# Performance work log

Measured on AMD Instinct MI355X. Metric: run time of the kernel, lower is better.

The kernel has to match this reference:

```python
import jax, jax.numpy as jnp
import numpy as np

N = 50000   # nodes
E = 800000  # edges (avg degree 16)
R = 3       # relations (distance bins)
IN = 3      # node_input_dim
H = 64      # hidden_dim
EA = 6      # edge_input_dim
DH = 32     # decoder_hidden_dim


def setup_inputs() -> dict:
    key = jax.random.key(0)
    ks = jax.random.split(key, 16)
    x = jax.random.normal(ks[0], (N, IN), jnp.float32)
    edge_index = jax.random.randint(ks[1], (2, E), 0, N)
    edge_attr = jax.random.uniform(ks[2], (E, EA), dtype=jnp.float32)
    # scale log1p-distance column so edges span all 3 bins (thresholds ~8.52, ~9.21)
    edge_attr = edge_attr.at[:, 0].mul(12.0)
    p = lambda k, s: jax.random.normal(k, s, jnp.float32) * 0.1
    return dict(
        x=x, edge_index=edge_index, edge_attr=edge_attr,
        w0=p(ks[3], (R, IN, H)), root0=p(ks[4], (IN, H)), b0=jnp.zeros((H,), jnp.float32),
        w1=p(ks[5], (R, H, H)),  root1=p(ks[6], (H, H)),  b1=jnp.zeros((H,), jnp.float32),
        w2=p(ks[7], (R, H, H)),  root2=p(ks[8], (H, H)),  b2=jnp.zeros((H,), jnp.float32),
        ln_g0=jnp.ones((H,), jnp.float32), ln_b0=jnp.zeros((H,), jnp.float32),
        ln_g1=jnp.ones((H,), jnp.float32), ln_b1=jnp.zeros((H,), jnp.float32),
        ln_g2=jnp.ones((H,), jnp.float32), ln_b2=jnp.zeros((H,), jnp.float32),
        res_w=p(ks[9], (IN, H)), res_b=jnp.zeros((H,), jnp.float32),
        dec_w1=p(ks[10], (4 * H + EA, DH)), dec_b1=jnp.zeros((DH,), jnp.float32),
        dec_w2=p(ks[11], (DH, DH // 2)),    dec_b2=jnp.zeros((DH // 2,), jnp.float32),
        dec_w3=p(ks[12], (DH // 2, 1)),     dec_b3=jnp.zeros((1,), jnp.float32),
    )


def _layernorm(v, g, b, eps=1e-5):
    mu = v.mean(-1, keepdims=True)
    var = ((v - mu) ** 2).mean(-1, keepdims=True)
    return (v - mu) / jnp.sqrt(var + eps) * g + b


def reference(x, edge_index, edge_attr,
              w0, root0, b0, w1, root1, b1, w2, root2, b2,
              ln_g0, ln_b0, ln_g1, ln_b1, ln_g2, ln_b2,
              res_w, res_b,
              dec_w1, dec_b1, dec_w2, dec_b2, dec_w3, dec_b3):
    dist = edge_attr[:, 0]
    q1 = jnp.log1p(jnp.float32(5000.0))
    q2 = jnp.log1p(jnp.float32(10000.0))
    edge_type = (dist > q1).astype(jnp.int32) + (dist > q2).astype(jnp.int32)  # [E]
    src, dst = edge_index[0], edge_index[1]

    def rgcn(xi, W, root, b):
        # RGCNConv with per-relation mean aggregation:
        # out_i = root x_i + b + sum_r W_r * mean_{j in N_r(i)} x_j
        # aggregate-then-transform: segment-sum masked source feats, divide by
        # per-relation in-degree, then one small [in,H] matmul per relation.
        xs = xi[src]                                  # [E, in] gather
        out = xi @ root + b                           # [N, H]
        for r in range(R):
            m = (edge_type == r).astype(xi.dtype)[:, None]
            s = jax.ops.segment_sum(xs * m, dst, num_segments=N)   # [N, in]
            c = jax.ops.segment_sum(m, dst, num_segments=N)        # [N, 1]
            out = out + (s / jnp.maximum(c, 1.0)) @ W[r]
        return out

    # encoder (eval mode -> dropout is identity)
    h = jax.nn.relu(rgcn(x, w0, root0, b0))
    h1 = _layernorm(h + x @ res_w + res_b, ln_g0, ln_b0)
    h = jax.nn.relu(rgcn(h1, w1, root1, b1))
    h2 = _layernorm(h + h1, ln_g1, ln_b1)
    h = jax.nn.relu(rgcn(h2, w2, root2, b2))
    h3 = _layernorm(h + h2, ln_g2, ln_b2)

    # edge decoder
    hs, hd = h3[src], h3[dst]                         # [E, H] gathers
    dec_in = jnp.concatenate([hs, hd, jnp.abs(hs - hd), hs * hd, edge_attr], axis=-1)
    z = jax.nn.relu(dec_in @ dec_w1 + dec_b1)
    z = jax.nn.relu(z @ dec_w2 + dec_b2)
    return (z @ dec_w3 + dec_b3).squeeze(-1)          # [E]
```

## Files before the change

kernel.cpp:

```cpp
#include <hip/hip_runtime.h>
#include <math.h>

#define NN 50000
#define NE 800000
#define HD 64
#define NB 196
#define NBK 196
#define BSE 2048
#define DT 5

typedef float f32x4 __attribute__((ext_vector_type(4)));
typedef float f32x16 __attribute__((ext_vector_type(16)));
typedef short short8 __attribute__((ext_vector_type(8)));
typedef _Float16 hf2 __attribute__((ext_vector_type(2)));
typedef _Float16 half8 __attribute__((ext_vector_type(8)));

__device__ __forceinline__ float wave_sum(float v) {
  #pragma unroll
  for (int off = 32; off > 0; off >>= 1) v += __shfl_xor(v, off, 64);
  return v;
}

__device__ __forceinline__ unsigned f2h_pk(float a, float b) {
  auto v = __builtin_amdgcn_cvt_pkrtz(a, b);
  union { decltype(v) h; unsigned u; } cv; cv.h = v; return cv.u;
}
__device__ __forceinline__ unsigned short f2h(float a) {
  union { _Float16 h; unsigned short u; } cv; cv.h = (_Float16)a; return cv.u;
}
__device__ __forceinline__ float h2f(unsigned short b) {
  union { unsigned short u; _Float16 h; } v; v.u = b; return (float)v.h;
}

__global__ __launch_bounds__(256) void bucket_count(
    const int* __restrict__ ei, int* __restrict__ bcnt)
{
  __shared__ int h[NBK];
  for (int i = threadIdx.x; i < NBK; i += 256) h[i] = 0;
  __syncthreads();
  int e0 = blockIdx.x * BSE;
  #pragma unroll
  for (int k = 0; k < BSE / 256; k++) {
    int e = e0 + k * 256 + threadIdx.x;
    if (e < NE) atomicAdd(&h[ei[NE + e] >> 8], 1);
  }
  __syncthreads();
  for (int i = threadIdx.x; i < NBK; i += 256)
    if (h[i]) atomicAdd(&bcnt[i], h[i]);
}

__global__ __launch_bounds__(256) void bucket_scan(
    const int* __restrict__ bcnt, int* __restrict__ bbase, int* __restrict__ bcur)
{
  __shared__ int sd[256];
  int v = (threadIdx.x < NBK) ? bcnt[threadIdx.x] : 0;
  sd[threadIdx.x] = v;
  __syncthreads();
  for (int s = 1; s < 256; s <<= 1) {
    int t = (threadIdx.x >= s) ? sd[threadIdx.x - s] : 0;
    __syncthreads();
    sd[threadIdx.x] += t;
    __syncthreads();
  }
  if (threadIdx.x < NBK) {
    int ex = sd[threadIdx.x] - v;
    bbase[threadIdx.x] = ex;
    bcur[threadIdx.x] = ex;
  }
  if (threadIdx.x == 0) bbase[NBK] = NE;
}

__global__ __launch_bounds__(256) void bucket_scatter(
    const int* __restrict__ ei, const float* __restrict__ ea,
    int* __restrict__ bcur, unsigned* __restrict__ recs)
{
  __shared__ int hcnt[NBK], hbase[NBK];
  for (int i = threadIdx.x; i < NBK; i += 256) hcnt[i] = 0;
  __syncthreads();
  const float q1 = log1pf(5000.0f);
  const float q2 = log1pf(10000.0f);
  int e0 = blockIdx.x * BSE;
  unsigned rec[BSE / 256];
  int bk[BSE / 256];
  #pragma unroll
  for (int k = 0; k < BSE / 256; k++) {
    int e = e0 + k * 256 + threadIdx.x;
    bk[k] = -1;
    if (e < NE) {
      int s = ei[e], d = ei[NE + e];
      float dist = ea[(size_t)e * 6];
      int r = (dist > q1 ? 1 : 0) + (dist > q2 ? 1 : 0);
      rec[k] = (unsigned)s | ((unsigned)(d & 255) << 16) | ((unsigned)r << 24);
      bk[k] = d >> 8;
      atomicAdd(&hcnt[bk[k]], 1);
    }
  }
  __syncthreads();
  for (int i = threadIdx.x; i < NBK; i += 256) {
    hbase[i] = hcnt[i] ? atomicAdd(&bcur[i], hcnt[i]) : 0;
    hcnt[i] = 0;
  }
  __syncthreads();
  #pragma unroll
  for (int k = 0; k < BSE / 256; k++) {
    if (bk[k] >= 0) {
      int idx = atomicAdd(&hcnt[bk[k]], 1);
      recs[hbase[bk[k]] + idx] = rec[k];
    }
  }
}

__global__ __launch_bounds__(256) void bucket_hist(
    const unsigned* __restrict__ recs, const int* __restrict__ bbase,
    int* __restrict__ cntR)
{
  __shared__ int h[768];
  for (int i = threadIdx.x; i < 768; i += 256) h[i] = 0;
  __syncthreads();
  int b = blockIdx.x;
  int lo = bbase[b], hi = bbase[b + 1];
  for (int i = lo + threadIdx.x; i < hi; i += 256) {
    unsigned rec = recs[i];
    int dlow = (rec >> 16) & 255, r = (rec >> 24) & 3;
    atomicAdd(&h[dlow * 3 + r], 1);
  }
  __syncthreads();
  for (int i = threadIdx.x; i < 768; i += 256) {
    int n = b * 256 + i / 3;
    if (n < NN) cntR[n * 3 + i % 3] = h[i];
  }
}

__global__ __launch_bounds__(256) void bucket_place(
    const unsigned* __restrict__ recs, const int* __restrict__ bbase,
    const int* __restrict__ off3, unsigned short* __restrict__ sorted)
{
  __shared__ int cur[768];
  int b = blockIdx.x;
  for (int i = threadIdx.x; i < 768; i += 256) {
    int n = b * 256 + i / 3;
    cur[i] = (n < NN) ? off3[n * 3 + i % 3] : 0;
  }
  __syncthreads();
  int lo = bbase[b], hi = bbase[b + 1];
  for (int i = lo + threadIdx.x; i < hi; i += 256) {
    unsigned rec = recs[i];
    int s = rec & 0xFFFF, dlow = (rec >> 16) & 255, r = (rec >> 24) & 3;
    int pos = atomicAdd(&cur[dlow * 3 + r], 1);
    sorted[pos] = (unsigned short)s;
  }
}

__global__ __launch_bounds__(256) void scanA(const int* __restrict__ cntR, int* __restrict__ bsum) {
  __shared__ int sd[256];
  int n = blockIdx.x * 256 + threadIdx.x;
  int deg = 0;
  if (n < NN) deg = cntR[3 * n] + cntR[3 * n + 1] + cntR[3 * n + 2];
  sd[threadIdx.x] = deg;
  __syncthreads();
  #pragma unroll
  for (int s = 128; s > 0; s >>= 1) {
    if (threadIdx.x < s) sd[threadIdx.x] += sd[threadIdx.x + s];
    __syncthreads();
  }
  if (threadIdx.x == 0) bsum[blockIdx.x] = sd[0];
}

__global__ __launch_bounds__(256) void scanB(int* __restrict__ bsum) {
  __shared__ int sd[256];
  int v = (threadIdx.x < NB) ? bsum[threadIdx.x] : 0;
  sd[threadIdx.x] = v;
  __syncthreads();
  for (int s = 1; s < 256; s <<= 1) {
    int t = (threadIdx.x >= s) ? sd[threadIdx.x - s] : 0;
    __syncthreads();
    sd[threadIdx.x] += t;
    __syncthreads();
  }
  if (threadIdx.x < NB) bsum[threadIdx.x] = sd[threadIdx.x] - v;
}

__global__ __launch_bounds__(256) void scanC(
    const int* __restrict__ cntR, const int* __restrict__ bsum,
    int* __restrict__ off3, float* __restrict__ dinv)
{
  __shared__ int sd[256];
  int n = blockIdx.x * 256 + threadIdx.x;
  int c0 = 0, c1 = 0, c2 = 0;
  if (n < NN) { c0 = cntR[3 * n]; c1 = cntR[3 * n + 1]; c2 = cntR[3 * n + 2]; }
  int deg = c0 + c1 + c2;
  sd[threadIdx.x] = deg;
  __syncthreads();
  for (int s = 1; s < 256; s <<= 1) {
    int t = (threadIdx.x >= s) ? sd[threadIdx.x - s] : 0;
    __syncthreads();
    sd[threadIdx.x] += t;
    __syncthreads();
  }
  if (n < NN) {
    int o = bsum[blockIdx.x] + sd[threadIdx.x] - deg;
    off3[3 * n + 0] = o;
    off3[3 * n + 1] = o + c0;
    off3[3 * n + 2] = o + c0 + c1;
    dinv[3 * n + 0] = 1.0f / (float)(c0 > 1 ? c0 : 1);
    dinv[3 * n + 1] = 1.0f / (float)(c1 > 1 ? c1 : 1);
    dinv[3 * n + 2] = 1.0f / (float)(c2 > 1 ? c2 : 1);
  }
}

__global__ __launch_bounds__(256) void agg0_pack(
    const float* __restrict__ x, const int* __restrict__ off3, const int* __restrict__ cntR,
    const unsigned short* __restrict__ sorted, float* __restrict__ agg0,
    const float* __restrict__ W1, const float* __restrict__ W2,
    const float* __restrict__ root1, const float* __restrict__ w1,
    const float* __restrict__ root2, const float* __restrict__ w2,
    unsigned short* __restrict__ pk3, unsigned short* __restrict__ pk2,
    unsigned short* __restrict__ pkl1, unsigned short* __restrict__ pkl2)
{
  if (blockIdx.x < 3) {
    if (blockIdx.x == 0) {
      for (int idx = threadIdx.x; idx < 8704; idx += 256) {
        int j = idx & 7, l = (idx >> 3) & 63, t = idx >> 9;
        int k = 16 * t + 8 * (l >> 5) + j;
        int n = l & 31;
        pk3[idx] = (k < 262) ? f2h(W1[k * 32 + n]) : (unsigned short)0;
      }
      for (int idx = threadIdx.x; idx < 512; idx += 256) {
        int j = idx & 7, l = idx >> 3;
        int k = (l >> 4) * 8 + j, n = l & 15;
        pk2[idx] = f2h(W2[k * 16 + n]);
      }
    } else {
      const float* root = (blockIdx.x == 1) ? root1 : root2;
      const float* W    = (blockIdx.x == 1) ? w1 : w2;
      unsigned short* pkL = (blockIdx.x == 1) ? pkl1 : pkl2;
      for (int idx = threadIdx.x; idx < 16384; idx += 256) {
        int j = idx & 7, l = (idx >> 3) & 63, nt = (idx >> 9) & 3, t = idx >> 11;
        int k = t * 32 + (l >> 4) * 8 + j;
        int n = nt * 16 + (l & 15);
        float w = (k < 64) ? root[k * 64 + n]
                           : W[((k - 64) >> 6) * 4096 + (k & 63) * 64 + n];
        pkL[idx] = f2h(w);
      }
    }
    return;
  }
  int wid = ((blockIdx.x - 3) * blockDim.x + threadIdx.x) >> 6;
  int lane = threadIdx.x & 63;
  int n = wid * 16 + (lane >> 2);
  int f = lane & 3;
  if (n >= NN) return;
  #pragma unroll
  for (int r = 0; r < 3; r++) {
    int st = off3[3 * n + r], len = cntR[3 * n + r];
    float a = 0.f;
    int i = 0;
    for (; i + 4 <= len; i += 4) {
      int s0 = sorted[st + i], s1 = sorted[st + i + 1];
      int s2 = sorted[st + i + 2], s3 = sorted[st + i + 3];
      float v0 = (f < 3) ? x[s0 * 3 + f] : 0.f;
      float v1 = (f < 3) ? x[s1 * 3 + f] : 0.f;
      float v2 = (f < 3) ? x[s2 * 3 + f] : 0.f;
      float v3 = (f < 3) ? x[s3 * 3 + f] : 0.f;
      a += (v0 + v1) + (v2 + v3);
    }
    for (; i < len; i++) {
      int s0 = sorted[st + i];
      a += (f < 3) ? x[s0 * 3 + f] : 0.f;
    }
    if (f < 3) agg0[n * 9 + r * 3 + f] = a;
  }
}

__global__ __launch_bounds__(256) void node0_kernel(
    const float* __restrict__ x, const float* __restrict__ agg0, const float* __restrict__ dinv,
    const float* __restrict__ w0, const float* __restrict__ root0, const float* __restrict__ b0,
    const float* __restrict__ res_w, const float* __restrict__ res_b,
    const float* __restrict__ g, const float* __restrict__ bb,
    unsigned short* __restrict__ hb)
{
  int wid = __builtin_amdgcn_readfirstlane((int)((blockIdx.x * blockDim.x + threadIdx.x) >> 6));
  int lane = threadIdx.x & 63;
  int n0 = wid * 8;
  if (n0 >= NN) return;
  float wr[3], ww[9], wres[3];
  #pragma unroll
  for (int i = 0; i < 3; i++) { wr[i] = root0[i * HD + lane]; wres[i] = res_w[i * HD + lane]; }
  #pragma unroll
  for (int i = 0; i < 9; i++) ww[i] = w0[i * HD + lane];
  float vb = b0[lane], vrb = res_b[lane], vg = g[lane], vbb = bb[lane];
  #pragma unroll
  for (int k = 0; k < 8; k++) {
    int nk = n0 + k;
    float xv[3];
    #pragma unroll
    for (int i = 0; i < 3; i++) xv[i] = x[nk * 3 + i];
    float v = vb;
    #pragma unroll
    for (int i = 0; i < 3; i++) v = fmaf(xv[i], wr[i], v);
    #pragma unroll
    for (int r = 0; r < 3; r++) {
      float s = 0.f;
      #pragma unroll
      for (int i = 0; i < 3; i++) s = fmaf(agg0[nk * 9 + r * 3 + i], ww[r * 3 + i], s);
      v = fmaf(dinv[nk * 3 + r], s, v);
    }
    v = fmaxf(v, 0.f);
    float res = vrb;
    #pragma unroll
    for (int i = 0; i < 3; i++) res = fmaf(xv[i], wres[i], res);
    float t = v + res;
    float mu = wave_sum(t) * 0.015625f;
    float dt = t - mu;
    float var = wave_sum(dt * dt) * 0.015625f;
    float o = dt * rsqrtf(var + 1e-5f) * vg + vbb;
    hb[(size_t)nk * HD + lane] = f2h(o);
  }
}

__global__ __launch_bounds__(256) void layer_fused(
    const unsigned short* __restrict__ hb_in, const unsigned short* __restrict__ pkL,
    const float* __restrict__ bias, const float* __restrict__ g, const float* __restrict__ bb,
    const int* __restrict__ off3, const int* __restrict__ cntR,
    const unsigned short* __restrict__ sorted, const float* __restrict__ dinv,
    unsigned short* __restrict__ hb_out)
{
  __shared__ unsigned short tile[4][16][256];
  int wv = threadIdx.x >> 6;
  int lane = threadIdx.x & 63;
  int wid = (blockIdx.x * blockDim.x + threadIdx.x) >> 6;
  int n0 = wid * 16;
  if (n0 >= NN) return;
  char* T = (char*)&tile[wv][0][0];

  {
    int m = lane >> 2;
    int q = lane & 3;
    int node = n0 + m;
    int swz = (m & 7) << 4;
    const unsigned short* hrow = hb_in + (size_t)node * HD + q * 16;
    uint4 rv0 = *(const uint4*)(hrow);
    uint4 rv1 = *(const uint4*)(hrow + 8);
    *(uint4*)(T + m * 512 + ((q * 32) ^ swz))      = rv0;
    *(uint4*)(T + m * 512 + ((q * 32 + 16) ^ swz)) = rv1;

    union U4 { uint4 u; hf2 h[4]; };
    #pragma unroll
    for (int r = 0; r < 3; r++) {
      int st = off3[node * 3 + r];
      int len = cntR[node * 3 + r];
      hf2 acc[8];
      #pragma unroll
      for (int j = 0; j < 8; j++) acc[j] = (hf2){(_Float16)0.f, (_Float16)0.f};
      int i = 0;
      for (; i + 4 <= len; i += 4) {
        int s0 = sorted[st + i],     s1 = sorted[st + i + 1];
        int s2 = sorted[st + i + 2], s3 = sorted[st + i + 3];
        const uint4* p0 = (const uint4*)(hb_in + (size_t)s0 * HD + q * 16);
        const uint4* p1 = (const uint4*)(hb_in + (size_t)s1 * HD + q * 16);
        const uint4* p2 = (const uint4*)(hb_in + (size_t)s2 * HD + q * 16);
        const uint4* p3 = (const uint4*)(hb_in + (size_t)s3 * HD + q * 16);
        U4 a0, a1, b0, b1, c0, c1, d0, d1;
        a0.u = p0[0]; a1.u = p0[1];
        b0.u = p1[0]; b1.u = p1[1];
        c0.u = p2[0]; c1.u = p2[1];
        d0.u = p3[0]; d1.u = p3[1];
        #pragma unroll
        for (int k = 0; k < 4; k++) {
          acc[k]     += (a0.h[k] + b0.h[k]) + (c0.h[k] + d0.h[k]);
          acc[4 + k] += (a1.h[k] + b1.h[k]) + (c1.h[k] + d1.h[k]);
        }
      }
      for (; i < len; i++) {
        int s0 = sorted[st + i];
        const uint4* p0 = (const uint4*)(hb_in + (size_t)s0 * HD + q * 16);
        U4 u0, u1;
        u0.u = p0[0]; u1.u = p0[1];
        #pragma unroll
        for (int k = 0; k < 4; k++) {
          acc[k]     += u0.h[k];
          acc[4 + k] += u1.h[k];
        }
      }
      float dv = dinv[node * 3 + r];
      unsigned pk[8];
      #pragma unroll
      for (int j = 0; j < 8; j++)
        pk[j] = f2h_pk((float)acc[j][0] * dv, (float)acc[j][1] * dv);
      uint4 w0 = make_uint4(pk[0], pk[1], pk[2], pk[3]);
      uint4 w1 = make_uint4(pk[4], pk[5], pk[6], pk[7]);
      *(uint4*)(T + m * 512 + ((128 + r * 128 + q * 32) ^ swz))      = w0;
      *(uint4*)(T + m * 512 + ((128 + r * 128 + q * 32 + 16) ^ swz)) = w1;
    }
  }

  asm volatile("s_waitcnt lgkmcnt(0)" ::: "memory");
  __builtin_amdgcn_sched_barrier(0);

  int m2 = lane & 15, gq = lane >> 4;
  int swz2 = (m2 & 7) << 4;
  const half8* Bp = (const half8*)pkL;
  f32x4 acc[4];
  #pragma unroll
  for (int nt = 0; nt < 4; nt++) acc[nt] = (f32x4){0.f, 0.f, 0.f, 0.f};
  #pragma unroll
  for (int t = 0; t < 8; t++) {
    union AF { short8 s; half8 h; } af;
    af.s = *(const short8*)(T + m2 * 512 + ((gq * 16 + t * 64) ^ swz2));
    #pragma unroll
    for (int nt = 0; nt < 4; nt++)
      acc[nt] = __builtin_amdgcn_mfma_f32_16x16x32_f16(af.h, Bp[(t * 4 + nt) * 64 + lane], acc[nt], 0, 0, 0);
  }

  float bias_v[4], g_v[4], bb_v[4];
  #pragma unroll
  for (int nt = 0; nt < 4; nt++) {
    bias_v[nt] = bias[nt * 16 + m2];
    g_v[nt] = g[nt * 16 + m2];
    bb_v[nt] = bb[nt * 16 + m2];
  }
  #pragma unroll
  for (int rr = 0; rr < 4; rr++) {
    int lrow = gq * 4 + rr;
    int nodeo = n0 + lrow;
    int swzr = (lrow & 7) << 4;
    float tv[4], s = 0.f;
    #pragma unroll
    for (int nt = 0; nt < 4; nt++) {
      unsigned short rh = *(const unsigned short*)(T + lrow * 512 + (((nt * 16 + m2) * 2) ^ swzr));
      float res = h2f(rh);
      float v = fmaxf(acc[nt][rr] + bias_v[nt], 0.f) + res;
      tv[nt] = v; s += v;
    }
    #pragma unroll
    for (int o = 1; o < 16; o <<= 1) s += __shfl_xor(s, o, 64);
    float mu = s * 0.015625f;
    float s2 = 0.f;
    #pragma unroll
    for (int nt = 0; nt < 4; nt++) { float dd = tv[nt] - mu; s2 += dd * dd; }
    #pragma unroll
    for (int o = 1; o < 16; o <<= 1) s2 += __shfl_xor(s2, o, 64);
    float rstd = rsqrtf(s2 * 0.015625f + 1e-5f);
    #pragma unroll
    for (int nt = 0; nt < 4; nt++) {
      float o = (tv[nt] - mu) * rstd * g_v[nt] + bb_v[nt];
      hb_out[(size_t)nodeo * HD + nt * 16 + m2] = f2h(o);
    }
  }
}

__global__ __launch_bounds__(256) void decoder_mfma(
    const unsigned short* __restrict__ hb, const int* __restrict__ ei, const float* __restrict__ ea,
    const unsigned short* __restrict__ pk3, const unsigned short* __restrict__ pk2,
    const float* __restrict__ B1, const float* __restrict__ B2,
    const float* __restrict__ W3, const float* __restrict__ B3,
    float* __restrict__ out)
{
  __shared__ float Zl[4 * 32 * 33];
  __shared__ unsigned short Bsh[8704 + 512];
  {
    unsigned* dsh = (unsigned*)Bsh;
    const unsigned* sp3 = (const unsigned*)pk3;
    for (int i = threadIdx.x; i < 4352; i += 256) dsh[i] = sp3[i];
    const unsigned* sp2 = (const unsigned*)pk2;
    if (threadIdx.x < 256) dsh[4352 + threadIdx.x] = sp2[threadIdx.x];
  }
  __syncthreads();

  int wv = threadIdx.x >> 6;
  int lane = threadIdx.x & 63;
  int r = lane & 31, u = lane >> 5;
  int base = (blockIdx.x * 4 + wv) * 32 * DT;

  int m = lane & 15, g = lane >> 4;
  float b1v = B1[r];
  float bias2 = B2[m];
  float w3v = W3[m];
  float b3v = B3[0];
  float* Z = Zl + wv * 1056;
  const half8* Bp  = (const half8*)Bsh;
  const half8* Bp2 = (const half8*)(Bsh + 8704);

  union u8h { short8 s8; half8 h8; hf2 h[4]; unsigned w[4]; };

  u8h hsA[4], hdA[4], hsB[4], hdB[4];
  float2 E0[3], E1[3], E2[3];

  auto GATH = [&](u8h* Hs, u8h* Hd, int s, int d) {
    const unsigned short* ps = hb + (size_t)s * HD + u * 8;
    const unsigned short* pq = hb + (size_t)d * HD + u * 8;
    #pragma unroll
    for (int t = 0; t < 4; t++) {
      Hs[t].s8 = *(const short8*)(ps + t * 16);
      Hd[t].s8 = *(const short8*)(pq + t * 16);
    }
  };
  auto LDEA = [&](float2* E, int e0t) {
    if (u == 0) {
      const float* er = ea + (size_t)(e0t + r) * 6;
      E[0] = *(const float2*)(er);
      E[1] = *(const float2*)(er + 2);
      E[2] = *(const float2*)(er + 4);
    }
  };
  auto COMP = [&](u8h* Hs, u8h* Hd, float2* E, int e0t) {
    u8h ad[4], pd[4];
    #pragma unroll
    for (int t = 0; t < 4; t++) {
      #pragma unroll
      for (int k = 0; k < 4; k++) {
        union { hf2 h; unsigned u; } dd;
        dd.h = Hs[t].h[k] - Hd[t].h[k];
        ad[t].w[k] = dd.u & 0x7FFF7FFFu;
        pd[t].h[k] = Hs[t].h[k] * Hd[t].h[k];
      }
    }
    u8h aea;
    aea.w[0] = 0; aea.w[1] = 0; aea.w[2] = 0; aea.w[3] = 0;
    if (u == 0) {
      aea.w[0] = f2h_pk(E[0].x, E[0].y);
      aea.w[1] = f2h_pk(E[1].x, E[1].y);
      aea.w[2] = f2h_pk(E[2].x, E[2].y);
    }

    f32x16 acc = {0.f, 0.f, 0.f, 0.f, 0.f, 0.f, 0.f, 0.f,
                  0.f, 0.f, 0.f, 0.f, 0.f, 0.f, 0.f, 0.f};
    #pragma unroll
    for (int t = 0; t < 4; t++)
      acc = __builtin_amdgcn_mfma_f32_32x32x16_f16(Hs[t].h8, Bp[t * 64 + lane], acc, 0, 0, 0);
    #pragma unroll
    for (int t = 0; t < 4; t++)
      acc = __builtin_amdgcn_mfma_f32_32x32x16_f16(Hd[t].h8, Bp[(4 + t) * 64 + lane], acc, 0, 0, 0);
    #pragma unroll
    for (int t = 0; t < 4; t++)
      acc = __builtin_amdgcn_mfma_f32_32x32x16_f16(ad[t].h8, Bp[(8 + t) * 64 + lane], acc, 0, 0, 0);
    #pragma unroll
    for (int t = 0; t < 4; t++)
      acc = __builtin_amdgcn_mfma_f32_32x32x16_f16(pd[t].h8, Bp[(12 + t) * 64 + lane], acc, 0, 0, 0);
    acc = __builtin_amdgcn_mfma_f32_32x32x16_f16(aea.h8, Bp[16 * 64 + lane], acc, 0, 0, 0);

    #pragma unroll
    for (int i = 0; i < 16; i++) {
      int row = (i & 3) + 8 * (i >> 2) + 4 * u;
      Z[r * 33 + row] = fmaxf(acc[i] + b1v, 0.f);
    }

    #pragma unroll
    for (int q = 0; q < 2; q++) {
      u8h A2;
      #pragma unroll
      for (int j2 = 0; j2 < 4; j2++)
        A2.w[j2] = f2h_pk(Z[(g * 8 + 2 * j2) * 33 + q * 16 + m],
                          Z[(g * 8 + 2 * j2 + 1) * 33 + q * 16 + m]);
      f32x4 acc2 = {0.f, 0.f, 0.f, 0.f};
      acc2 = __builtin_amdgcn_mfma_f32_16x16x32_f16(A2.h8, Bp2[lane], acc2, 0, 0, 0);

      float t0 = fmaxf(acc2[0] + bias2, 0.f) * w3v;
      float t1 = fmaxf(acc2[1] + bias2, 0.f) * w3v;
      float t2 = fmaxf(acc2[2] + bias2, 0.f) * w3v;
      float t3 = fmaxf(acc2[3] + bias2, 0.f) * w3v;
      #pragma unroll
      for (int off = 1; off < 16; off <<= 1) {
        t0 += __shfl_xor(t0, off, 64);
        t1 += __shfl_xor(t1, off, 64);
        t2 += __shfl_xor(t2, off, 64);
        t3 += __shfl_xor(t3, off, 64);
      }
      if (m < 4) {
        float val = (m == 0) ? t0 : (m == 1) ? t1 : (m == 2) ? t2 : t3;
        out[e0t + q * 16 + g * 4 + m] = val + b3v;
      }
    }
  };

  int s1, d1;
  {
    int s0 = ei[base + r], d0 = ei[NE + base + r];
    LDEA(E0, base);
    GATH(hsA, hdA, s0, d0);
  }
  s1 = ei[base + 32 + r]; d1 = ei[NE + base + 32 + r];
  LDEA(E1, base + 32);

  #pragma unroll
  for (int t = 0; t < DT; t++) {
    if (t + 1 < DT) GATH(hsB, hdB, s1, d1);
    int s2 = 0, d2 = 0;
    if (t + 2 < DT) {
      s2 = ei[base + (t + 2) * 32 + r]; d2 = ei[NE + base + (t + 2) * 32 + r];
      LDEA(E2, base + (t + 2) * 32);
    }
    COMP(hsA, hdA, E0, base + t * 32);
    #pragma unroll
    for (int k = 0; k < 4; k++) { hsA[k] = hsB[k]; hdA[k] = hdB[k]; }
    E0[0] = E1[0]; E0[1] = E1[1]; E0[2] = E1[2];
    E1[0] = E2[0]; E1[1] = E2[1]; E1[2] = E2[2];
    s1 = s2; d1 = d2;
  }
}

extern "C" void kernel_launch(void* const* d_in, const int* in_sizes, int n_in,
                              void* d_out, int out_size, void* d_ws, size_t ws_size,
                              hipStream_t stream) {
  const float* x      = (const float*)d_in[0];
  const int*   ei     = (const int*)d_in[1];
  const float* ea     = (const float*)d_in[2];
  const float* w0     = (const float*)d_in[3];
  const float* root0  = (const float*)d_in[4];
  const float* b0     = (const float*)d_in[5];
  const float* w1     = (const float*)d_in[6];
  const float* root1  = (const float*)d_in[7];
  const float* b1     = (const float*)d_in[8];
  const float* w2     = (const float*)d_in[9];
  const float* root2  = (const float*)d_in[10];
  const float* b2     = (const float*)d_in[11];
  const float* ln_g0  = (const float*)d_in[12];
  const float* ln_b0  = (const float*)d_in[13];
  const float* ln_g1  = (const float*)d_in[14];
  const float* ln_b1  = (const float*)d_in[15];
  const float* ln_g2  = (const float*)d_in[16];
  const float* ln_b2  = (const float*)d_in[17];
  const float* res_w  = (const float*)d_in[18];
  const float* res_b  = (const float*)d_in[19];
  const float* dec_w1 = (const float*)d_in[20];
  const float* dec_b1 = (const float*)d_in[21];
  const float* dec_w2 = (const float*)d_in[22];
  const float* dec_b2 = (const float*)d_in[23];
  const float* dec_w3 = (const float*)d_in[24];
  const float* dec_b3 = (const float*)d_in[25];

  char* ws = (char*)d_ws;
  unsigned* recs = (unsigned*)(ws + 0);
  int*   bcnt    = (int*)(ws + 3200000);
  int*   bbase   = (int*)(ws + 3201024);
  int*   bcur    = (int*)(ws + 3202048);
  float* agg0    = (float*)(ws + 3203072);
  int*   bsum    = (int*)(ws + 5003072);
  int*   off3    = (int*)(ws + 5004096);
  float* dinv    = (float*)(ws + 5604096);
  int*   cntR    = (int*)(ws + 6204096);
  unsigned short* sorted = (unsigned short*)(ws + 6804096);
  unsigned short* pk3  = (unsigned short*)(ws + 8404096);
  unsigned short* pkw2 = (unsigned short*)(ws + 8421504);
  unsigned short* pkl1 = (unsigned short*)(ws + 8422528);
  unsigned short* pkl2 = (unsigned short*)(ws + 8455296);
  unsigned short* hb   = (unsigned short*)(ws + 8488064);
  unsigned short* hb2  = (unsigned short*)(ws + 14888064);

  hipMemsetAsync(bcnt, 0, 1024, stream);

  const int sort_blocks = (NE + BSE - 1) / BSE;

  bucket_count<<<sort_blocks, 256, 0, stream>>>(ei, bcnt);
  bucket_scan<<<1, 256, 0, stream>>>(bcnt, bbase, bcur);
  bucket_scatter<<<sort_blocks, 256, 0, stream>>>(ei, ea, bcur, recs);
  bucket_hist<<<NBK, 256, 0, stream>>>(recs, bbase, cntR);
  scanA<<<NB, 256, 0, stream>>>(cntR, bsum);
  scanB<<<1, 256, 0, stream>>>(bsum);
  scanC<<<NB, 256, 0, stream>>>(cntR, bsum, off3, dinv);
  bucket_place<<<NBK, 256, 0, stream>>>(recs, bbase, off3, sorted);

  agg0_pack<<<3 + (NN + 63) / 64, 256, 0, stream>>>(x, off3, cntR, sorted, agg0,
                                                    dec_w1, dec_w2, root1, w1, root2, w2,
                                                    pk3, pkw2, pkl1, pkl2);

  const int node0_blocks = (NN / 8 + 3) / 4;
  const int fused_blocks = (NN / 16 + 3) / 4;

  node0_kernel<<<node0_blocks, 256, 0, stream>>>(x, agg0, dinv, w0, root0, b0,
                                                 res_w, res_b, ln_g0, ln_b0, hb);

  layer_fused<<<fused_blocks, 256, 0, stream>>>(hb, pkl1, b1, ln_g1, ln_b1,
                                                off3, cntR, sorted, dinv, hb2);
  layer_fused<<<fused_blocks, 256, 0, stream>>>(hb2, pkl2, b2, ln_g2, ln_b2,
                                                off3, cntR, sorted, dinv, hb);

  decoder_mfma<<<NE / (128 * DT), 256, 0, stream>>>(hb, ei, ea, pk3, pkw2, dec_b1,
                                                    dec_b2, dec_w3, dec_b3, (float*)d_out);
}
```

Before: 273.8 us.

## Fuse CSR build kernels, widen gather unroll, store decoder hidden as fp16

Merges bucket_hist, three scan kernels and bucket_place into one kernel per bucket. Each bucket computes a local prefix sum offset from the bucket base, which removes four launches and the global scan round-trips. The neighbour-aggregation loop in layer_fused now issues 8 gathers per iteration instead of 4, to raise memory-level parallelism. The decoder stores its first hidden layer in LDS as packed fp16 instead of fp32, with a launch-bounds occupancy hint, to cut LDS traffic and conversions; the wider unroll may add register pressure.

```diff
diff --git a/kernel.cpp b/kernel.cpp
--- a/kernel.cpp
+++ b/kernel.cpp
@@ -4,7 +4,6 @@
 #define NN 50000
 #define NE 800000
 #define HD 64
-#define NB 196
 #define NBK 196
 #define BSE 2048
 #define DT 5
@@ -110,101 +109,54 @@
   }
 }
 
-__global__ __launch_bounds__(256) void bucket_hist(
+__global__ __launch_bounds__(256) void bucket_histplace(
     const unsigned* __restrict__ recs, const int* __restrict__ bbase,
-    int* __restrict__ cntR)
+    int* __restrict__ cntR, int* __restrict__ off3, float* __restrict__ dinv,
+    unsigned short* __restrict__ sorted)
 {
   __shared__ int h[768];
-  for (int i = threadIdx.x; i < 768; i += 256) h[i] = 0;
-  __syncthreads();
+  __shared__ int cur[768];
+  __shared__ int ts[256];
   int b = blockIdx.x;
+  int t = threadIdx.x;
+  for (int i = t; i < 768; i += 256) h[i] = 0;
+  __syncthreads();
   int lo = bbase[b], hi = bbase[b + 1];
-  for (int i = lo + threadIdx.x; i < hi; i += 256) {
+  for (int i = lo + t; i < hi; i += 256) {
     unsigned rec = recs[i];
-    int dlow = (rec >> 16) & 255, r = (rec >> 24) & 3;
-    atomicAdd(&h[dlow * 3 + r], 1);
-  }
-  __syncthreads();
-  for (int i = threadIdx.x; i < 768; i += 256) {
-    int n = b * 256 + i / 3;
-    if (n < NN) cntR[n * 3 + i % 3] = h[i];
-  }
-}
-
-__global__ __launch_bounds__(256) void bucket_place(
-    const unsigned* __restrict__ recs, const int* __restrict__ bbase,
-    const int* __restrict__ off3, unsigned short* __restrict__ sorted)
-{
-  __shared__ int cur[768];
-  int b = blockIdx.x;
-  for (int i = threadIdx.x; i < 768; i += 256) {
-    int n = b * 256 + i / 3;
-    cur[i] = (n < NN) ? off3[n * 3 + i % 3] : 0;
-  }
-  __syncthreads();
-  int lo = bbase[b], hi = bbase[b + 1];
-  for (int i = lo + threadIdx.x; i < hi; i += 256) {
+    atomicAdd(&h[((rec >> 16) & 255) * 3 + ((rec >> 24) & 3)], 1);
+  }
+  __syncthreads();
+  int s0 = h[3 * t], s1 = h[3 * t + 1], s2 = h[3 * t + 2];
+  int tot = s0 + s1 + s2;
+  ts[t] = tot;
+  __syncthreads();
+  for (int s = 1; s < 256; s <<= 1) {
+    int v = (t >= s) ? ts[t - s] : 0;
+    __syncthreads();
+    ts[t] += v;
+    __syncthreads();
+  }
+  int base = lo + ts[t] - tot;
+  int n = b * 256 + t;
+  if (n < NN) {
+    off3[3 * n + 0] = base;
+    off3[3 * n + 1] = base + s0;
+    off3[3 * n + 2] = base + s0 + s1;
+    cntR[3 * n + 0] = s0;
+    cntR[3 * n + 1] = s1;
+    cntR[3 * n + 2] = s2;
+    dinv[3 * n + 0] = 1.0f / (float)(s0 > 1 ? s0 : 1);
+    dinv[3 * n + 1] = 1.0f / (float)(s1 > 1 ? s1 : 1);
+    dinv[3 * n + 2] = 1.0f / (float)(s2 > 1 ? s2 : 1);
+  }
+  cur[3 * t] = base; cur[3 * t + 1] = base + s0; cur[3 * t + 2] = base + s0 + s1;
+  __syncthreads();
+  for (int i = lo + t; i < hi; i += 256) {
     unsigned rec = recs[i];
-    int s = rec & 0xFFFF, dlow = (rec >> 16) & 255, r = (rec >> 24) & 3;
-    int pos = atomicAdd(&cur[dlow * 3 + r], 1);
-    sorted[pos] = (unsigned short)s;
-  }
-}
-
-__global__ __launch_bounds__(256) void scanA(const int* __restrict__ cntR, int* __restrict__ bsum) {
-  __shared__ int sd[256];
-  int n = blockIdx.x * 256 + threadIdx.x;
-  int deg = 0;
-  if (n < NN) deg = cntR[3 * n] + cntR[3 * n + 1] + cntR[3 * n + 2];
-  sd[threadIdx.x] = deg;
-  __syncthreads();
-  #pragma unroll
-  for (int s = 128; s > 0; s >>= 1) {
-    if (threadIdx.x < s) sd[threadIdx.x] += sd[threadIdx.x + s];
-    __syncthreads();
-  }
-  if (threadIdx.x == 0) bsum[blockIdx.x] = sd[0];
-}
-
-__global__ __launch_bounds__(256) void scanB(int* __restrict__ bsum) {
-  __shared__ int sd[256];
-  int v = (threadIdx.x < NB) ? bsum[threadIdx.x] : 0;
-  sd[threadIdx.x] = v;
-  __syncthreads();
-  for (int s = 1; s < 256; s <<= 1) {
-    int t = (threadIdx.x >= s) ? sd[threadIdx.x - s] : 0;
-    __syncthreads();
-    sd[threadIdx.x] += t;
-    __syncthreads();
-  }
-  if (threadIdx.x < NB) bsum[threadIdx.x] = sd[threadIdx.x] - v;
-}
-
-__global__ __launch_bounds__(256) void scanC(
-    const int* __restrict__ cntR, const int* __restrict__ bsum,
-    int* __restrict__ off3, float* __restrict__ dinv)
-{
-  __shared__ int sd[256];
-  int n = blockIdx.x * 256 + threadIdx.x;
-  int c0 = 0, c1 = 0, c2 = 0;
-  if (n < NN) { c0 = cntR[3 * n]; c1 = cntR[3 * n + 1]; c2 = cntR[3 * n + 2]; }
-  int deg = c0 + c1 + c2;
-  sd[threadIdx.x] = deg;
-  __syncthreads();
-  for (int s = 1; s < 256; s <<= 1) {
-    int t = (threadIdx.x >= s) ? sd[threadIdx.x - s] : 0;
-    __syncthreads();
-    sd[threadIdx.x] += t;
-    __syncthreads();
-  }
-  if (n < NN) {
-    int o = bsum[blockIdx.x] + sd[threadIdx.x] - deg;
-    off3[3 * n + 0] = o;
-    off3[3 * n + 1] = o + c0;
-    off3[3 * n + 2] = o + c0 + c1;
-    dinv[3 * n + 0] = 1.0f / (float)(c0 > 1 ? c0 : 1);
-    dinv[3 * n + 1] = 1.0f / (float)(c1 > 1 ? c1 : 1);
-    dinv[3 * n + 2] = 1.0f / (float)(c2 > 1 ? c2 : 1);
+    int idx = ((rec >> 16) & 255) * 3 + ((rec >> 24) & 3);
+    int pos = atomicAdd(&cur[idx], 1);
+    sorted[pos] = (unsigned short)(rec & 0xFFFF);
   }
 }
 
@@ -353,25 +305,37 @@
       #pragma unroll
       for (int j = 0; j < 8; j++) acc[j] = (hf2){(_Float16)0.f, (_Float16)0.f};
       int i = 0;
-      for (; i + 4 <= len; i += 4) {
-        int s0 = sorted[st + i],     s1 = sorted[st + i + 1];
-        int s2 = sorted[st + i + 2], s3 = sorted[st + i + 3];
+      for (; i + 8 <= len; i += 8) {
+        int ss[8];
+        #pragma unroll
+        for (int j = 0; j < 8; j++) ss[j] = sorted[st + i + j];
+        U4 lo[8], hiw[8];
+        #pragma unroll
+        for (int j = 0; j < 8; j++) {
+          const uint4* p = (const uint4*)(hb_in + (size_t)ss[j] * HD + q * 16);
+          lo[j].u = p[0]; hiw[j].u = p[1];
+        }
+        #pragma unroll
+        for (int k = 0; k < 4; k++) {
+          acc[k]     += ((lo[0].h[k] + lo[1].h[k]) + (lo[2].h[k] + lo[3].h[k]))
+                      + ((lo[4].h[k] + lo[5].h[k]) + (lo[6].h[k] + lo[7].h[k]));
+          acc[4 + k] += ((hiw[0].h[k] + hiw[1].h[k]) + (hiw[2].h[k] + hiw[3].h[k]))
+                      + ((hiw[4].h[k] + hiw[5].h[k]) + (hiw[6].h[k] + hiw[7].h[k]));
+        }
+      }
+      for (; i + 2 <= len; i += 2) {
+        int s0 = sorted[st + i], s1 = sorted[st + i + 1];
         const uint4* p0 = (const uint4*)(hb_in + (size_t)s0 * HD + q * 16);
         const uint4* p1 = (const uint4*)(hb_in + (size_t)s1 * HD + q * 16);
-        const uint4* p2 = (const uint4*)(hb_in + (size_t)s2 * HD + q * 16);
-        const uint4* p3 = (const uint4*)(hb_in + (size_t)s3 * HD + q * 16);
-        U4 a0, a1, b0, b1, c0, c1, d0, d1;
-        a0.u = p0[0]; a1.u = p0[1];
-        b0.u = p1[0]; b1.u = p1[1];
-        c0.u = p2[0]; c1.u = p2[1];
-        d0.u = p3[0]; d1.u = p3[1];
+        U4 a0, a1, b0, b1;
+        a0.u = p0[0]; a1.u = p0[1]; b0.u = p1[0]; b1.u = p1[1];
         #pragma unroll
         for (int k = 0; k < 4; k++) {
-          acc[k]     += (a0.h[k] + b0.h[k]) + (c0.h[k] + d0.h[k]);
-          acc[4 + k] += (a1.h[k] + b1.h[k]) + (c1.h[k] + d1.h[k]);
+          acc[k]     += a0.h[k] + b0.h[k];
+          acc[4 + k] += a1.h[k] + b1.h[k];
         }
       }
-      for (; i < len; i++) {
+      if (i < len) {
         int s0 = sorted[st + i];
         const uint4* p0 = (const uint4*)(hb_in + (size_t)s0 * HD + q * 16);
         U4 u0, u1;
@@ -449,14 +413,14 @@
   }
 }
 
-__global__ __launch_bounds__(256) void decoder_mfma(
+__global__ __launch_bounds__(256, 5) void decoder_mfma(
     const unsigned short* __restrict__ hb, const int* __restrict__ ei, const float* __restrict__ ea,
     const unsigned short* __restrict__ pk3, const unsigned short* __restrict__ pk2,
     const float* __restrict__ B1, const float* __restrict__ B2,
     const float* __restrict__ W3, const float* __restrict__ B3,
     float* __restrict__ out)
 {
-  __shared__ float Zl[4 * 32 * 33];
+  __shared__ unsigned short Zl16[4 * 32 * 34];
   __shared__ unsigned short Bsh[8704 + 512];
   {
     unsigned* dsh = (unsigned*)Bsh;
@@ -477,7 +441,7 @@
   float bias2 = B2[m];
   float w3v = W3[m];
   float b3v = B3[0];
-  float* Z = Zl + wv * 1056;
+  unsigned short* Z16 = Zl16 + wv * 1088;
   const half8* Bp  = (const half8*)Bsh;
   const half8* Bp2 = (const half8*)(Bsh + 8704);
 
@@ -540,18 +504,25 @@
     acc = __builtin_amdgcn_mfma_f32_32x32x16_f16(aea.h8, Bp[16 * 64 + lane], acc, 0, 0, 0);
 
     #pragma unroll
-    for (int i = 0; i < 16; i++) {
-      int row = (i & 3) + 8 * (i >> 2) + 4 * u;
-      Z[r * 33 + row] = fmaxf(acc[i] + b1v, 0.f);
-    }
+    for (int k = 0; k < 4; k++) {
+      unsigned w0 = f2h_pk(fmaxf(acc[4 * k + 0] + b1v, 0.f), fmaxf(acc[4 * k + 1] + b1v, 0.f));
+      unsigned w1 = f2h_pk(fmaxf(acc[4 * k + 2] + b1v, 0.f), fmaxf(acc[4 * k + 3] + b1v, 0.f));
+      *(unsigned*)(Z16 + r * 34 + 8 * k + 4 * u)     = w0;
+      *(unsigned*)(Z16 + r * 34 + 8 * k + 4 * u + 2) = w1;
+    }
+    asm volatile("s_waitcnt lgkmcnt(0)" ::: "memory");
+    __builtin_amdgcn_sched_barrier(0);
 
     #pragma unroll
     for (int q = 0; q < 2; q++) {
       u8h A2;
       #pragma unroll
-      for (int j2 = 0; j2 < 4; j2++)
-        A2.w[j2] = f2h_pk(Z[(g * 8 + 2 * j2) * 33 + q * 16 + m],
-                          Z[(g * 8 + 2 * j2 + 1) * 33 + q * 16 + m]);
+      for (int j2 = 0; j2 < 4; j2++) {
+        int e0 = g * 8 + 2 * j2, cc = q * 16 + m;
+        unsigned lo = Z16[e0 * 34 + cc];
+        unsigned hi = Z16[(e0 + 1) * 34 + cc];
+        A2.w[j2] = lo | (hi << 16);
+      }
       f32x4 acc2 = {0.f, 0.f, 0.f, 0.f};
       acc2 = __builtin_amdgcn_mfma_f32_16x16x32_f16(A2.h8, Bp2[lane], acc2, 0, 0, 0);
 
@@ -635,7 +606,6 @@
   int*   bbase   = (int*)(ws + 3201024);
   int*   bcur    = (int*)(ws + 3202048);
   float* agg0    = (float*)(ws + 3203072);
-  int*   bsum    = (int*)(ws + 5003072);
   int*   off3    = (int*)(ws + 5004096);
   float* dinv    = (float*)(ws + 5604096);
   int*   cntR    = (int*)(ws + 6204096);
@@ -654,11 +624,7 @@
   bucket_count<<<sort_blocks, 256, 0, stream>>>(ei, bcnt);
   bucket_scan<<<1, 256, 0, stream>>>(bcnt, bbase, bcur);
   bucket_scatter<<<sort_blocks, 256, 0, stream>>>(ei, ea, bcur, recs);
-  bucket_hist<<<NBK, 256, 0, stream>>>(recs, bbase, cntR);
-  scanA<<<NB, 256, 0, stream>>>(cntR, bsum);
-  scanB<<<1, 256, 0, stream>>>(bsum);
-  scanC<<<NB, 256, 0, stream>>>(cntR, bsum, off3, dinv);
-  bucket_place<<<NBK, 256, 0, stream>>>(recs, bbase, off3, sorted);
+  bucket_histplace<<<NBK, 256, 0, stream>>>(recs, bbase, cntR, off3, dinv, sorted);
 
   agg0_pack<<<3 + (NN + 63) / 64, 256, 0, stream>>>(x, off3, cntR, sorted, agg0,
                                                     dec_w1, dec_w2, root1, w1, root2, w2,
```

New measurement: 321.7 us. 17.5% more time.
